# Optimization experiments

Measured on AMD Instinct MI355X. Metric: run time of the kernel, lower is better.

The kernel has to match this reference:

```python
import jax, jax.numpy as jnp
import numpy as np

B, NF, S, L, H, MID, KS, NC, DENSE = 16, 8, 16, 256, 128, 32, 8, 10, 512
COEFF = 0.1
BN_EPS = 1e-5


def _normalize(x):
    return x / jnp.maximum(jnp.linalg.norm(x, axis=-1, keepdims=True), 1e-12)


def _sparsemax(z):
    # sparsemax over last axis (Martins & Astudillo 2016)
    zs = jnp.flip(jnp.sort(z, axis=-1), axis=-1)
    k = jnp.arange(1, z.shape[-1] + 1, dtype=z.dtype)
    cum = jnp.cumsum(zs, axis=-1)
    support = (1.0 + k * zs) > cum
    ksup = jnp.sum(support, axis=-1, keepdims=True)
    tau = (jnp.take_along_axis(cum, ksup - 1, axis=-1) - 1.0) / ksup.astype(z.dtype)
    return jnp.maximum(z - tau, 0.0)


def _bn_ncl(x, g, b, m, v):  # eval-mode BatchNorm1d on [N, C, L]
    return g[None, :, None] * (x - m[None, :, None]) * jax.lax.rsqrt(v[None, :, None] + BN_EPS) + b[None, :, None]


def _bn_nc(x, g, b, m, v):  # eval-mode BatchNorm1d on [N, C]
    return g * (x - m) * jax.lax.rsqrt(v + BN_EPS) + b


def _conv(x, w, pad):
    return jax.lax.conv_general_dilated(x, w, (1,), [(pad, pad)], dimension_numbers=('NCH', 'OIH', 'NCH'))


def _maxpool2(x):  # MaxPool1d(kernel=2, stride=2, padding=1): -inf padded
    return jax.lax.reduce_window(x, -jnp.inf, jax.lax.max, (1, 1, 2), (1, 1, 2), ((0, 0), (0, 0), (1, 1)))


def _cnn(x, cw1, bn1, cw2, bn2, cw3, bn3):
    x = _maxpool2(jax.nn.relu(_bn_ncl(_conv(x, cw1, KS // 2), *bn1)))
    x = _maxpool2(jax.nn.relu(_bn_ncl(_conv(x, cw2, 4), *bn2)))
    x = _maxpool2(jax.nn.relu(_bn_ncl(_conv(x, cw3, 4), *bn3)))
    return jnp.mean(x, axis=-1)  # AdaptiveAvgPool1d(1) -> [N, H]


def _alpha_beta(x, cw1, bn1, cw2, bn2, cw3, bn3, Wq, bq, Wk, bk, Wv, bv):
    b = x.shape[0]
    xf = jnp.transpose(x, (1, 0, 2, 3)).reshape(NF, b * S, 1, L)
    rep = jax.vmap(_cnn)(xf, cw1, bn1, cw2, bn2, cw3, bn3)  # [F, B*S, H]
    rep = rep.reshape(NF, b, S, H)
    Q = jax.nn.elu(rep @ Wq + bq)
    K = jax.nn.leaky_relu(rep @ Wk + bk)
    V = jax.nn.leaky_relu(rep @ Wv + bv)
    # mean_t(Q @ K^T) == Q @ mean_t(K); then scale by sqrt(d_k)
    scores = jnp.einsum('fbsh,fbh->fbs', Q, jnp.mean(K, axis=2)) / jnp.sqrt(jnp.float32(H))
    intra_aw = _sparsemax(scores)                             # [F, B, S]
    Z = _normalize(jnp.einsum('fbs,fbsh->fbh', intra_aw, V))  # [F, B, H]
    Kn = _normalize(rep)
    inter_scores = jnp.einsum('ibh,fbsh->ifbs', Z, Kn)        # cosine scores (Z already unit-norm)
    inter_aw = _sparsemax(inter_scores)                       # [I, F, B, S]
    U = jnp.einsum('ifbs,fbsh->ibh', inter_aw, rep) / NF      # mean over feature axis f
    Hc = _normalize(jnp.concatenate([Z, U], axis=-1))         # [F, B, 2H]
    feat = jnp.transpose(Hc, (1, 0, 2)).reshape(b, NF * 2 * H)
    return feat, intra_aw, inter_aw


def _forward(src_x, src_y, tgt_x, cw1, bn1_g, bn1_b, bn1_m, bn1_v, cw2, bn2_g, bn2_b, bn2_m, bn2_v, cw3, bn3_g, bn3_b, bn3_m, bn3_v, Wq, bq, Wk, bk, Wv, bv, bnc1_g, bnc1_b, bnc1_m, bnc1_v, W1, b1, bnc2_g, bnc2_b, bnc2_m, bnc2_v, W2, b2):
    bn1 = (bn1_g, bn1_b, bn1_m, bn1_v)
    bn2 = (bn2_g, bn2_b, bn2_m, bn2_v)
    bn3 = (bn3_g, bn3_b, bn3_m, bn3_v)
    sf, sa, sb = _alpha_beta(src_x, cw1, bn1, cw2, bn2, cw3, bn3, Wq, bq, Wk, bk, Wv, bv)
    _, ta, tb = _alpha_beta(tgt_x, cw1, bn1, cw2, bn2, cw3, bn3, Wq, bq, Wk, bk, Wv, bv)
    h = _bn_nc(sf, bnc1_g, bnc1_b, bnc1_m, bnc1_v) @ W1 + b1
    h = jax.nn.leaky_relu(_bn_nc(h, bnc2_g, bnc2_b, bnc2_m, bnc2_v))
    y_pred = jax.nn.softmax(h @ W2 + b2, axis=-1)
    # MMD domain losses (detached in original via torch.tensor(list))
    da = jnp.mean(sa - ta, axis=-2)                           # [F, S]
    loss_a = COEFF * jnp.mean(jnp.linalg.norm(da, axis=-1))
    db = jnp.mean(sb - tb, axis=-2)                           # [I, F, S]
    loss_b = COEFF * jnp.mean(jnp.sqrt(jnp.sum(db * db, axis=(1, 2))))
    dom = jax.lax.stop_gradient(loss_a + loss_b)
    # CrossEntropyLoss applied to already-softmaxed preds, as in source
    logp = jax.nn.log_softmax(y_pred, axis=-1)
    ce = -jnp.mean(logp[jnp.arange(y_pred.shape[0]), src_y])
    return y_pred, ce + dom


def setup_inputs() -> dict:
    ks = jax.random.split(jax.random.key(0), 40)
    rn = lambda i, sh, s=1.0: s * jax.random.normal(ks[i], sh, dtype=jnp.float32)
    ru = lambda i, sh, lo, hi: jax.random.uniform(ks[i], sh, jnp.float32, lo, hi)
    return {
        'src_x': rn(0, (B, NF, S, L)),
        'src_y': jax.random.randint(ks[1], (B,), 0, NC),
        'tgt_x': rn(2, (B, NF, S, L)),
        'cw1': rn(3, (NF, MID, 1, KS), 0.1),
        'bn1_g': ru(4, (NF, MID), 0.75, 1.25), 'bn1_b': rn(5, (NF, MID), 0.1),
        'bn1_m': rn(6, (NF, MID), 0.1), 'bn1_v': ru(7, (NF, MID), 0.5, 1.5),
        'cw2': rn(8, (NF, 2 * MID, MID, 8), 0.05),
        'bn2_g': ru(9, (NF, 2 * MID), 0.75, 1.25), 'bn2_b': rn(10, (NF, 2 * MID), 0.1),
        'bn2_m': rn(11, (NF, 2 * MID), 0.1), 'bn2_v': ru(12, (NF, 2 * MID), 0.5, 1.5),
        'cw3': rn(13, (NF, H, 2 * MID, 8), 0.05),
        'bn3_g': ru(14, (NF, H), 0.75, 1.25), 'bn3_b': rn(15, (NF, H), 0.1),
        'bn3_m': rn(16, (NF, H), 0.1), 'bn3_v': ru(17, (NF, H), 0.5, 1.5),
        'Wq': rn(18, (H, H), 0.05), 'bq': rn(19, (H,), 0.02),
        'Wk': rn(20, (H, H), 0.05), 'bk': rn(21, (H,), 0.02),
        'Wv': rn(22, (H, H), 0.05), 'bv': rn(23, (H,), 0.02),
        'bnc1_g': ru(24, (NF * 2 * H,), 0.75, 1.25), 'bnc1_b': rn(25, (NF * 2 * H,), 0.1),
        'bnc1_m': rn(26, (NF * 2 * H,), 0.1), 'bnc1_v': ru(27, (NF * 2 * H,), 0.5, 1.5),
        'W1': rn(28, (NF * 2 * H, DENSE), 0.03), 'b1': rn(29, (DENSE,), 0.02),
        'bnc2_g': ru(30, (DENSE,), 0.75, 1.25), 'bnc2_b': rn(31, (DENSE,), 0.1),
        'bnc2_m': rn(32, (DENSE,), 0.1), 'bnc2_v': ru(33, (DENSE,), 0.5, 1.5),
        'W2': rn(34, (DENSE, NC), 0.05), 'b2': rn(35, (NC,), 0.02),
    }


def reference(src_x, src_y, tgt_x, cw1, bn1_g, bn1_b, bn1_m, bn1_v, cw2, bn2_g, bn2_b, bn2_m, bn2_v, cw3, bn3_g, bn3_b, bn3_m, bn3_v, Wq, bq, Wk, bk, Wv, bv, bnc1_g, bnc1_b, bnc1_m, bnc1_v, W1, b1, bnc2_g, bnc2_b, bnc2_m, bnc2_v, W2, b2):
    return _forward(src_x, src_y, tgt_x, cw1, bn1_g, bn1_b, bn1_m, bn1_v, cw2, bn2_g, bn2_b, bn2_m, bn2_v, cw3, bn3_g, bn3_b, bn3_m, bn3_v, Wq, bq, Wk, bk, Wv, bv, bnc1_g, bnc1_b, bnc1_m, bnc1_v, W1, b1, bnc2_g, bnc2_b, bnc2_m, bnc2_v, W2, b2)
```

## Files before the change

kernel.cpp:

```cpp
#include <hip/hip_runtime.h>

typedef unsigned short u16;
typedef unsigned int u32;
typedef __attribute__((ext_vector_type(8))) short bfrag;
typedef __attribute__((ext_vector_type(4))) float ffrag;

__device__ __forceinline__ float lrelu(float x) { return x >= 0.f ? x : 0.01f * x; }
__device__ __forceinline__ float eluf(float x)  { return x > 0.f ? x : expm1f(x); }
__device__ __forceinline__ u16 f2bf(float f) {
    u32 x = __float_as_uint(f);
    return (u16)((x + 0x7fffu + ((x >> 16) & 1u)) >> 16);
}
__device__ __forceinline__ float bf2f(u16 u) {
    return __uint_as_float(((u32)u) << 16);
}

__device__ void sparsemax16(const float* z, float* out) {
    float zs[16];
    for (int i = 0; i < 16; ++i) zs[i] = z[i];
    for (int i = 1; i < 16; ++i) {
        float key = zs[i]; int j = i - 1;
        while (j >= 0 && zs[j] < key) { zs[j + 1] = zs[j]; --j; }
        zs[j + 1] = key;
    }
    float cum[16];
    cum[0] = zs[0];
    for (int i = 1; i < 16; ++i) cum[i] = cum[i - 1] + zs[i];
    int ksup = 0;
    for (int k = 1; k <= 16; ++k)
        if (1.0f + (float)k * zs[k - 1] > cum[k - 1]) ksup++;
    if (ksup < 1) ksup = 1;
    float tau = (cum[ksup - 1] - 1.0f) / (float)ksup;
    for (int i = 0; i < 16; ++i) out[i] = fmaxf(z[i] - tau, 0.0f);
}

__global__ __launch_bounds__(256) void k_wprep(
    const float* __restrict__ w2, const float* __restrict__ w3,
    u16* __restrict__ wpk2, u16* __restrict__ wpk3)
{
    int i = blockIdx.x * 256 + threadIdx.x;
    if (i < 131072) {
        int j = i & 7, L = (i >> 3) & 63, kc = (i >> 9) & 7, nt = (i >> 12) & 3, f = i >> 14;
        int co = nt * 16 + (L & 15);
        int ci = ((L >> 4) << 3) + j;
        wpk2[i] = f2bf(w2[(((size_t)f * 64 + co) * 32 + ci) * 8 + kc]);
    } else if (i < 131072 + 524288) {
        int i2 = i - 131072;
        int j = i2 & 7, L = (i2 >> 3) & 63, kc = (i2 >> 9) & 15, nt = (i2 >> 13) & 7, f = i2 >> 16;
        int co = nt * 16 + (L & 15);
        int ci = ((kc & 1) << 5) + ((L >> 4) << 3) + j;
        wpk3[i2] = f2bf(w3[(((size_t)f * 128 + co) * 64 + ci) * 8 + (kc >> 1)]);
    }
}

#define S1T_STRIDE 40
#define S2T_STRIDE 72
#define RB_OFF 6336
#define SMEM_U16 15448

__global__ __launch_bounds__(256) void k_cnn(
    const float* __restrict__ xs, const float* __restrict__ xt,
    const float* __restrict__ w1, const float* __restrict__ g1, const float* __restrict__ b1,
    const float* __restrict__ m1, const float* __restrict__ v1,
    const float* __restrict__ g2, const float* __restrict__ b2,
    const float* __restrict__ m2, const float* __restrict__ v2,
    const float* __restrict__ g3, const float* __restrict__ b3,
    const float* __restrict__ m3, const float* __restrict__ v3,
    const u16* __restrict__ wpk2, const u16* __restrict__ wpk3,
    float* __restrict__ rep)
{
    __shared__ __align__(16) u16 smem[SMEM_U16];
    float* xin = (float*)(smem + RB_OFF);

    int tid = threadIdx.x, blk = blockIdx.x;
    int pass = blk >> 11, f = (blk >> 8) & 7, n = blk & 255;
    int bb = n >> 4, ss = n & 15;
    int lane = tid & 63, w = tid >> 6;
    const float* x = pass ? xt : xs;
    float* rep_p = rep + (size_t)pass * 262144;

    {
        u32* z = (u32*)smem;
        for (int i = tid; i < 3168; i += 256) z[i] = 0;
        for (int i = tid; i < 264; i += 256) xin[i] = 0.f;
    }
    __syncthreads();
    {
        const float* xr = x + (((size_t)bb * 8 + f) * 16 + ss) * 256;
        for (int i = tid; i < 256; i += 256) xin[i + 4] = xr[i];
    }
    __syncthreads();

    if (tid < 208) {
        int cc = tid & 7, jc = tid >> 3;
        int co0 = cc * 4, j0 = jc * 5;
        float wr[4][8];
        for (int c = 0; c < 4; ++c) {
            const float4* q = reinterpret_cast<const float4*>(w1 + ((size_t)f * 32 + co0 + c) * 8);
            float4 a = q[0], bq = q[1];
            wr[c][0] = a.x; wr[c][1] = a.y; wr[c][2] = a.z; wr[c][3] = a.w;
            wr[c][4] = bq.x; wr[c][5] = bq.y; wr[c][6] = bq.z; wr[c][7] = bq.w;
        }
        int px[10];
        for (int i = 0; i < 10; ++i) {
            int p = 2 * j0 - 1 + i;
            px[i] = p < 0 ? 0 : (p > 256 ? 256 : p);
        }
        float acc[4][10];
        for (int c = 0; c < 4; ++c) for (int i = 0; i < 10; ++i) acc[c][i] = 0.f;
        for (int k = 0; k < 8; ++k) {
            float xv[10];
            for (int i = 0; i < 10; ++i) xv[i] = xin[px[i] + k];
            for (int c = 0; c < 4; ++c)
                for (int i = 0; i < 10; ++i) acc[c][i] += wr[c][k] * xv[i];
        }
        for (int c = 0; c < 4; ++c) {
            int co = co0 + c;
            float sc = g1[f * 32 + co] * rsqrtf(v1[f * 32 + co] + 1e-5f);
            float sh = b1[f * 32 + co] - m1[f * 32 + co] * sc;
            for (int jj = 0; jj < 5; ++jj) {
                int j = j0 + jj;
                if (j < 129) {
                    float a0 = fmaxf(acc[c][2 * jj] * sc + sh, 0.f);
                    float a1 = fmaxf(acc[c][2 * jj + 1] * sc + sh, 0.f);
                    smem[(j + 4) * S1T_STRIDE + co] = f2bf(fmaxf(a0, a1));
                }
            }
        }
    }
    __syncthreads();

    {
        int nt = w;
        bfrag B2[8];
        const bfrag* gB = reinterpret_cast<const bfrag*>(wpk2);
        for (int kc = 0; kc < 8; ++kc)
            B2[kc] = gB[(((size_t)f * 4 + nt) * 8 + kc) * 64 + lane];
        int co = nt * 16 + (lane & 15);
        float sc = g2[f * 64 + co] * rsqrtf(v2[f * 64 + co] + 1e-5f);
        float sh = b2[f * 64 + co] - m2[f * 64 + co] * sc;
        int arow = lane & 15, ci0 = (lane >> 4) << 3;
        for (int mt = 0; mt < 9; ++mt) {
            ffrag C = {0.f, 0.f, 0.f, 0.f};
            int rb = mt * 16 + arow;
            for (int kc = 0; kc < 8; ++kc) {
                bfrag A = *reinterpret_cast<const bfrag*>(&smem[(rb + kc) * S1T_STRIDE + ci0]);
                C = __builtin_amdgcn_mfma_f32_16x16x32_bf16(A, B2[kc], C, 0, 0, 0);
            }
            int p0 = mt * 16 + ((lane >> 4) << 2);
            for (int r = 0; r < 4; ++r) {
                int p = p0 + r;
                if (p < 130)
                    smem[RB_OFF + p * 64 + co] = f2bf(fmaxf(C[r] * sc + sh, 0.f));
            }
        }
    }
    __syncthreads();

    {
        u32* z = (u32*)smem;
        for (int i = tid; i < 3168; i += 256) z[i] = 0;
    }
    __syncthreads();

    for (int e = tid; e < 66 * 64; e += 256) {
        int j = e >> 6, ci = e & 63;
        float vmax;
        if (j == 0) {
            vmax = bf2f(smem[RB_OFF + 0 * 64 + ci]);
        } else if (j == 65) {
            vmax = bf2f(smem[RB_OFF + 129 * 64 + ci]);
        } else {
            float a0 = bf2f(smem[RB_OFF + (2 * j - 1) * 64 + ci]);
            float a1 = bf2f(smem[RB_OFF + (2 * j) * 64 + ci]);
            vmax = fmaxf(a0, a1);
        }
        smem[(j + 4) * S2T_STRIDE + ci] = f2bf(vmax);
    }
    __syncthreads();

    for (int t = 0; t < 2; ++t) {
        int nt = w * 2 + t;
        bfrag B3[16];
        const bfrag* gB = reinterpret_cast<const bfrag*>(wpk3);
        for (int kc = 0; kc < 16; ++kc)
            B3[kc] = gB[(((size_t)f * 8 + nt) * 16 + kc) * 64 + lane];
        int co = nt * 16 + (lane & 15);
        float sc = g3[f * 128 + co] * rsqrtf(v3[f * 128 + co] + 1e-5f);
        float sh = b3[f * 128 + co] - m3[f * 128 + co] * sc;
        int arow = lane & 15, q8 = (lane >> 4) << 3;
        for (int mt = 0; mt < 5; ++mt) {
            ffrag C = {0.f, 0.f, 0.f, 0.f};
            int rb = mt * 16 + arow;
            for (int kc = 0; kc < 16; ++kc) {
                int row = rb + (kc >> 1);
                int ci0 = ((kc & 1) << 5) + q8;
                bfrag A = *reinterpret_cast<const bfrag*>(&smem[row * S2T_STRIDE + ci0]);
                C = __builtin_amdgcn_mfma_f32_16x16x32_bf16(A, B3[kc], C, 0, 0, 0);
            }
            int p0 = mt * 16 + ((lane >> 4) << 2);
            for (int r = 0; r < 4; ++r) {
                int p = p0 + r;
                if (p < 67)
                    smem[RB_OFF + p * 136 + co] = f2bf(fmaxf(C[r] * sc + sh, 0.f));
            }
        }
    }
    __syncthreads();

    if (tid < 128) {
        int co = tid;
        float sum = bf2f(smem[RB_OFF + 0 * 136 + co]);
        for (int j = 1; j < 34; ++j) {
            float a0 = bf2f(smem[RB_OFF + (2 * j - 1) * 136 + co]);
            float a1 = bf2f(smem[RB_OFF + (2 * j) * 136 + co]);
            sum += fmaxf(a0, a1);
        }
        rep_p[(((size_t)f * 256) + n) * 128 + co] = sum * (1.0f / 34.0f);
    }
}

__global__ __launch_bounds__(128) void k_attn1(
    const float* __restrict__ rep,
    const float* __restrict__ Wq, const float* __restrict__ bq,
    const float* __restrict__ Wk, const float* __restrict__ bk,
    const float* __restrict__ Wv, const float* __restrict__ bv,
    float* __restrict__ Zn, float* __restrict__ rninv, float* __restrict__ iaw)
{
    __shared__ float repL[2048], QL[2048], VL[2048];
    __shared__ float KmL[128], red[128], scoresL[16], awL[16];
    int tid = threadIdx.x;
    int pass = blockIdx.x >> 7, f = (blockIdx.x >> 4) & 7, b = blockIdx.x & 15;
    const float* rep_p = rep + (size_t)pass * 262144;
    float* Zn_p = Zn + (size_t)pass * 16384;
    float* rninv_p = rninv + (size_t)pass * 2048;
    float* iaw_p = iaw + (size_t)pass * 2048;

    const float* rb = rep_p + ((size_t)f * 256 + b * 16) * 128;
    for (int i = tid; i < 2048; i += 128) repL[i] = rb[i];
    __syncthreads();

    int h2 = tid;
    float km = 0.f;
    float bqv = bq[h2], bkv = bk[h2], bvv = bv[h2];
    for (int s0 = 0; s0 < 16; s0 += 8) {
        float aq[8], ak[8], av[8];
        for (int t = 0; t < 8; ++t) { aq[t] = bqv; ak[t] = bkv; av[t] = bvv; }
        for (int h = 0; h < 128; ++h) {
            float wq = Wq[h * 128 + h2];
            float wk = Wk[h * 128 + h2];
            float wv = Wv[h * 128 + h2];
            for (int t = 0; t < 8; ++t) {
                float r = repL[(s0 + t) * 128 + h];
                aq[t] += r * wq; ak[t] += r * wk; av[t] += r * wv;
            }
        }
        for (int t = 0; t < 8; ++t) {
            QL[(s0 + t) * 128 + h2] = eluf(aq[t]);
            VL[(s0 + t) * 128 + h2] = lrelu(av[t]);
            km += lrelu(ak[t]);
        }
    }
    KmL[h2] = km * (1.f / 16.f);
    __syncthreads();

    if (tid < 16) {
        float a = 0.f;
        for (int h = 0; h < 128; ++h) a += QL[tid * 128 + h] * KmL[h];
        scoresL[tid] = a * 0.08838834764831845f;
        float r2 = 0.f;
        for (int h = 0; h < 128; ++h) { float r = repL[tid * 128 + h]; r2 += r * r; }
        rninv_p[f * 256 + b * 16 + tid] = 1.f / fmaxf(sqrtf(r2), 1e-12f);
    }
    __syncthreads();
    if (tid == 0) sparsemax16(scoresL, awL);
    __syncthreads();
    if (tid < 16) iaw_p[f * 256 + b * 16 + tid] = awL[tid];

    float z = 0.f;
    for (int s = 0; s < 16; ++s) z += awL[s] * VL[s * 128 + tid];
    red[tid] = z * z;
    __syncthreads();
    for (int st = 64; st > 0; st >>= 1) {
        if (tid < st) red[tid] += red[tid + st];
        __syncthreads();
    }
    float inv = 1.f / fmaxf(sqrtf(red[0]), 1e-12f);
    Zn_p[((size_t)f * 16 + b) * 128 + tid] = z * inv;
}

__global__ __launch_bounds__(256) void k_attn2(
    const float* __restrict__ rep, const float* __restrict__ Zn,
    const float* __restrict__ rninv, float* __restrict__ ibw,
    const float* __restrict__ g, const float* __restrict__ bb,
    const float* __restrict__ mm, const float* __restrict__ vv,
    float* __restrict__ featbn)
{
    __shared__ float ZnL[1024], sc[1024], UL[1024], nrm[8];
    int tid = threadIdx.x;
    int pass = blockIdx.x >> 4, b = blockIdx.x & 15;
    const float* rep_p = rep + (size_t)pass * 262144;
    const float* Zn_p = Zn + (size_t)pass * 16384;
    const float* rninv_p = rninv + (size_t)pass * 2048;
    float* ibw_p = ibw + (size_t)pass * 16384;

    for (int i = tid; i < 1024; i += 256) {
        int ii = i >> 7, h = i & 127;
        ZnL[i] = Zn_p[((size_t)ii * 16 + b) * 128 + h];
    }
    if (tid < 8) nrm[tid] = 0.f;
    __syncthreads();

    for (int e = tid; e < 1024; e += 256) {
        int i = e >> 7, f = (e >> 4) & 7, s = e & 15;
        const float* rr = rep_p + ((size_t)f * 256 + b * 16 + s) * 128;
        float a = 0.f;
        for (int h = 0; h < 128; ++h) a += ZnL[i * 128 + h] * rr[h];
        sc[(i * 8 + f) * 16 + s] = a * rninv_p[f * 256 + b * 16 + s];
    }
    __syncthreads();
    if (tid < 64) {
        int i = tid >> 3, f = tid & 7;
        float aw[16];
        sparsemax16(&sc[(i * 8 + f) * 16], aw);
        for (int s = 0; s < 16; ++s) {
            sc[(i * 8 + f) * 16 + s] = aw[s];
            ibw_p[(((size_t)i * 8 + f) * 16 + b) * 16 + s] = aw[s];
        }
    }
    __syncthreads();
    if (pass == 0) {
        for (int e = tid; e < 1024; e += 256) {
            int i = e >> 7, h = e & 127;
            float u = 0.f;
            for (int f = 0; f < 8; ++f) {
                const float* rr = rep_p + ((size_t)f * 256 + b * 16) * 128 + h;
                const float* aa = &sc[(i * 8 + f) * 16];
                for (int s = 0; s < 16; ++s) u += aa[s] * rr[s * 128];
            }
            UL[e] = u * 0.125f;
        }
        __syncthreads();
        for (int e = tid; e < 1024; e += 256) {
            int f = e >> 7;
            float zz = ZnL[e], uu = UL[e];
            atomicAdd(&nrm[f], zz * zz + uu * uu);
        }
        __syncthreads();
        for (int e = tid; e < 2048; e += 256) {
            int f = e >> 8, d = e & 255;
            float inv = 1.f / fmaxf(sqrtf(nrm[f]), 1e-12f);
            float val = (d < 128 ? ZnL[f * 128 + d] : UL[f * 128 + d - 128]) * inv;
            float scv = g[e] * rsqrtf(vv[e] + 1e-5f);
            featbn[b * 2048 + e] = (val - mm[e]) * scv + bb[e];
        }
    }
}

__global__ __launch_bounds__(256) void k_head1(
    const float* __restrict__ featbn,
    const float* __restrict__ W1, const float* __restrict__ b1,
    const float* __restrict__ g2, const float* __restrict__ bb2,
    const float* __restrict__ mm2, const float* __restrict__ vv2,
    float* __restrict__ h2ws)
{
    __shared__ float featL[2048];
    __shared__ float part[8][32];
    int tid = threadIdx.x, blk = blockIdx.x;
    int b = blk >> 4, cc = blk & 15;
    for (int i = tid; i < 2048; i += 256) featL[i] = featbn[b * 2048 + i];
    __syncthreads();
    int ci = tid & 31, ks = tid >> 5;
    int col = cc * 32 + ci;
    const float* wcol = W1 + (size_t)(ks * 256) * 512 + col;
    const float* fl = featL + ks * 256;
    float a = 0.f;
    for (int c = 0; c < 256; ++c) a += fl[c] * wcol[(size_t)c * 512];
    part[ks][ci] = a;
    __syncthreads();
    if (tid < 32) {
        int colw = cc * 32 + tid;
        float s = b1[colw];
        for (int k2 = 0; k2 < 8; ++k2) s += part[k2][tid];
        float scv = g2[colw] * rsqrtf(vv2[colw] + 1e-5f);
        float val = (s - mm2[colw]) * scv + bb2[colw];
        h2ws[b * 512 + colw] = lrelu(val);
    }
}

__global__ __launch_bounds__(256) void k_tail(
    const float* __restrict__ h2ws,
    const float* __restrict__ W2, const float* __restrict__ b2,
    const float* __restrict__ sa, const float* __restrict__ ta,
    const float* __restrict__ sb, const float* __restrict__ tb,
    const int* __restrict__ sy, float* __restrict__ dout)
{
    __shared__ float h2L[8192];
    __shared__ float lgL[160], ypL[160];
    __shared__ float sA[8], sB[8];
    int tid = threadIdx.x;
    for (int i = tid; i < 8192; i += 256) h2L[i] = h2ws[i];
    if (tid < 8) { sA[tid] = 0.f; sB[tid] = 0.f; }
    __syncthreads();
    if (tid < 160) {
        int b = tid / 10, j = tid - b * 10;
        float a = b2[j];
        const float* h = h2L + b * 512;
        for (int c = 0; c < 512; ++c) a += h[c] * W2[c * 10 + j];
        lgL[tid] = a;
    }
    __syncthreads();
    if (tid < 16) {
        int b = tid;
        float mx = lgL[b * 10];
        for (int j = 1; j < 10; ++j) mx = fmaxf(mx, lgL[b * 10 + j]);
        float sum = 0.f, ex[10];
        for (int j = 0; j < 10; ++j) { ex[j] = expf(lgL[b * 10 + j] - mx); sum += ex[j]; }
        for (int j = 0; j < 10; ++j) {
            float p = ex[j] / sum;
            ypL[b * 10 + j] = p;
            dout[b * 10 + j] = p;
        }
    }
    __syncthreads();
    if (tid < 128) {
        int f = tid >> 4, s = tid & 15;
        float d = 0.f;
        for (int b = 0; b < 16; ++b) d += sa[f * 256 + b * 16 + s] - ta[f * 256 + b * 16 + s];
        d *= (1.f / 16.f);
        atomicAdd(&sA[f], d * d);
    }
    for (int e = tid; e < 1024; e += 256) {
        int i = e >> 7, f = (e >> 4) & 7, s = e & 15;
        float d = 0.f;
        int base = ((i * 8 + f) * 16) * 16 + s;
        for (int b = 0; b < 16; ++b) d += sb[base + b * 16] - tb[base + b * 16];
        d *= (1.f / 16.f);
        atomicAdd(&sB[i], d * d);
    }
    __syncthreads();
    if (tid == 0) {
        float la = 0.f, lb = 0.f;
        for (int f = 0; f < 8; ++f) la += sqrtf(sA[f]);
        for (int i = 0; i < 8; ++i) lb += sqrtf(sB[i]);
        la *= 0.1f / 8.f;
        lb *= 0.1f / 8.f;
        float ce = 0.f;
        for (int b = 0; b < 16; ++b) {
            const float* y = ypL + b * 10;
            float mx = y[0];
            for (int j = 1; j < 10; ++j) mx = fmaxf(mx, y[j]);
            float sum = 0.f;
            for (int j = 0; j < 10; ++j) sum += expf(y[j] - mx);
            float lse = mx + logf(sum);
            ce += lse - y[sy[b]];
        }
        ce *= (1.f / 16.f);
        dout[160] = ce + la + lb;
    }
}

extern "C" void kernel_launch(void* const* d_in, const int* in_sizes, int n_in,
                              void* d_out, int out_size, void* d_ws, size_t ws_size,
                              hipStream_t stream) {
    (void)in_sizes; (void)n_in; (void)out_size; (void)ws_size;
    const float* src_x = (const float*)d_in[0];
    const int*   src_y = (const int*)d_in[1];
    const float* tgt_x = (const float*)d_in[2];
    const float *cw1 = (const float*)d_in[3], *bn1g = (const float*)d_in[4],
                *bn1b = (const float*)d_in[5], *bn1m = (const float*)d_in[6],
                *bn1v = (const float*)d_in[7];
    const float *cw2 = (const float*)d_in[8], *bn2g = (const float*)d_in[9],
                *bn2b = (const float*)d_in[10], *bn2m = (const float*)d_in[11],
                *bn2v = (const float*)d_in[12];
    const float *cw3 = (const float*)d_in[13], *bn3g = (const float*)d_in[14],
                *bn3b = (const float*)d_in[15], *bn3m = (const float*)d_in[16],
                *bn3v = (const float*)d_in[17];
    const float *Wq = (const float*)d_in[18], *bq = (const float*)d_in[19],
                *Wk = (const float*)d_in[20], *bk = (const float*)d_in[21],
                *Wv = (const float*)d_in[22], *bv = (const float*)d_in[23];
    const float *bc1g = (const float*)d_in[24], *bc1b = (const float*)d_in[25],
                *bc1m = (const float*)d_in[26], *bc1v = (const float*)d_in[27];
    const float *W1 = (const float*)d_in[28], *b1 = (const float*)d_in[29];
    const float *bc2g = (const float*)d_in[30], *bc2b = (const float*)d_in[31],
                *bc2m = (const float*)d_in[32], *bc2v = (const float*)d_in[33];
    const float *W2 = (const float*)d_in[34], *b2 = (const float*)d_in[35];

    float* ws = (float*)d_ws;
    size_t o = 0;
    float* rep    = ws + o; o += (size_t)2 * 262144;
    float* Zn     = ws + o; o += (size_t)2 * 16384;
    float* rninv  = ws + o; o += (size_t)2 * 2048;
    float* ia     = ws + o; o += (size_t)2 * 2048;
    float* ib     = ws + o; o += (size_t)2 * 16384;
    float* featbn = ws + o; o += (size_t)16 * 2048;
    float* h2ws   = ws + o; o += (size_t)16 * 512;
    u16* wpk2 = (u16*)(ws + o); o += 65536;
    u16* wpk3 = (u16*)(ws + o); o += 262144;

    k_wprep<<<2560, 256, 0, stream>>>(cw2, cw3, wpk2, wpk3);
    k_cnn<<<4096, 256, 0, stream>>>(src_x, tgt_x,
        cw1, bn1g, bn1b, bn1m, bn1v,
        bn2g, bn2b, bn2m, bn2v,
        bn3g, bn3b, bn3m, bn3v,
        wpk2, wpk3, rep);
    k_attn1<<<256, 128, 0, stream>>>(rep, Wq, bq, Wk, bk, Wv, bv, Zn, rninv, ia);
    k_attn2<<<32, 256, 0, stream>>>(rep, Zn, rninv, ib, bc1g, bc1b, bc1m, bc1v, featbn);
    k_head1<<<256, 256, 0, stream>>>(featbn, W1, b1, bc2g, bc2b, bc2m, bc2v, h2ws);
    k_tail<<<1, 256, 0, stream>>>(h2ws, W2, b2, ia, ia + 2048, ib, ib + 16384,
                                  src_y, (float*)d_out);
}
```

Measured before the change: 352.6 us.

## Use bf16 MFMA for QKV projections, pad CNN LDS strides, truncate bf16 conversion

The attention kernel's Q/K/V projections move from scalar FP32 loops to bf16 MFMA. The weights are prepacked into fragment layout in the weight-prep kernel, and reductions use wave shuffles instead of shared-memory trees. The CNN's intermediate LDS buffers get padded strides to cut bank conflicts. Round-to-nearest bf16 conversion is replaced with plain truncation, which is cheaper but adds precision loss in the projections and CNN activations.

```diff
diff --git a/kernel.cpp b/kernel.cpp
--- a/kernel.cpp
+++ b/kernel.cpp
@@ -10,6 +10,9 @@
 __device__ __forceinline__ u16 f2bf(float f) {
     u32 x = __float_as_uint(f);
     return (u16)((x + 0x7fffu + ((x >> 16) & 1u)) >> 16);
+}
+__device__ __forceinline__ u16 f2bt(float f) {
+    return (u16)(__float_as_uint(f) >> 16);
 }
 __device__ __forceinline__ float bf2f(u16 u) {
     return __uint_as_float(((u32)u) << 16);
@@ -36,7 +39,9 @@
 
 __global__ __launch_bounds__(256) void k_wprep(
     const float* __restrict__ w2, const float* __restrict__ w3,
-    u16* __restrict__ wpk2, u16* __restrict__ wpk3)
+    const float* __restrict__ Wq, const float* __restrict__ Wk,
+    const float* __restrict__ Wv,
+    u16* __restrict__ wpk2, u16* __restrict__ wpk3, u16* __restrict__ wqkv)
 {
     int i = blockIdx.x * 256 + threadIdx.x;
     if (i < 131072) {
@@ -50,13 +55,23 @@
         int co = nt * 16 + (L & 15);
         int ci = ((kc & 1) << 5) + ((L >> 4) << 3) + j;
         wpk3[i2] = f2bf(w3[(((size_t)f * 128 + co) * 64 + ci) * 8 + (kc >> 1)]);
+    } else if (i < 131072 + 524288 + 49152) {
+        int j2 = i - 655360;
+        int proj = j2 >> 14, idx = j2 & 16383;
+        int jj = idx & 7, L = (idx >> 3) & 63, kc = (idx >> 9) & 3, nt = idx >> 11;
+        int n = nt * 16 + (L & 15);
+        int k = kc * 32 + ((L >> 4) << 3) + jj;
+        const float* W = proj == 0 ? Wq : (proj == 1 ? Wk : Wv);
+        wqkv[j2] = f2bf(W[k * 128 + n]);
     }
 }
 
 #define S1T_STRIDE 40
 #define S2T_STRIDE 72
+#define RB2_STRIDE 68
+#define RB3_STRIDE 140
 #define RB_OFF 6336
-#define SMEM_U16 15448
+#define SMEM_U16 (RB_OFF + 67 * RB3_STRIDE)
 
 __global__ __launch_bounds__(256) void k_cnn(
     const float* __restrict__ xs, const float* __restrict__ xt,
@@ -123,7 +138,7 @@
                 if (j < 129) {
                     float a0 = fmaxf(acc[c][2 * jj] * sc + sh, 0.f);
                     float a1 = fmaxf(acc[c][2 * jj + 1] * sc + sh, 0.f);
-                    smem[(j + 4) * S1T_STRIDE + co] = f2bf(fmaxf(a0, a1));
+                    smem[(j + 4) * S1T_STRIDE + co] = f2bt(fmaxf(a0, a1));
                 }
             }
         }
@@ -151,7 +166,7 @@
             for (int r = 0; r < 4; ++r) {
                 int p = p0 + r;
                 if (p < 130)
-                    smem[RB_OFF + p * 64 + co] = f2bf(fmaxf(C[r] * sc + sh, 0.f));
+                    smem[RB_OFF + p * RB2_STRIDE + co] = f2bt(fmaxf(C[r] * sc + sh, 0.f));
             }
         }
     }
@@ -167,15 +182,15 @@
         int j = e >> 6, ci = e & 63;
         float vmax;
         if (j == 0) {
-            vmax = bf2f(smem[RB_OFF + 0 * 64 + ci]);
+            vmax = bf2f(smem[RB_OFF + 0 * RB2_STRIDE + ci]);
         } else if (j == 65) {
-            vmax = bf2f(smem[RB_OFF + 129 * 64 + ci]);
+            vmax = bf2f(smem[RB_OFF + 129 * RB2_STRIDE + ci]);
         } else {
-            float a0 = bf2f(smem[RB_OFF + (2 * j - 1) * 64 + ci]);
-            float a1 = bf2f(smem[RB_OFF + (2 * j) * 64 + ci]);
+            float a0 = bf2f(smem[RB_OFF + (2 * j - 1) * RB2_STRIDE + ci]);
+            float a1 = bf2f(smem[RB_OFF + (2 * j) * RB2_STRIDE + ci]);
             vmax = fmaxf(a0, a1);
         }
-        smem[(j + 4) * S2T_STRIDE + ci] = f2bf(vmax);
+        smem[(j + 4) * S2T_STRIDE + ci] = f2bt(vmax);
     }
     __syncthreads();
 
@@ -202,7 +217,7 @@
             for (int r = 0; r < 4; ++r) {
                 int p = p0 + r;
                 if (p < 67)
-                    smem[RB_OFF + p * 136 + co] = f2bf(fmaxf(C[r] * sc + sh, 0.f));
+                    smem[RB_OFF + p * RB3_STRIDE + co] = f2bt(fmaxf(C[r] * sc + sh, 0.f));
             }
         }
     }
@@ -210,83 +225,130 @@
 
     if (tid < 128) {
         int co = tid;
-        float sum = bf2f(smem[RB_OFF + 0 * 136 + co]);
+        float sum = bf2f(smem[RB_OFF + 0 * RB3_STRIDE + co]);
         for (int j = 1; j < 34; ++j) {
-            float a0 = bf2f(smem[RB_OFF + (2 * j - 1) * 136 + co]);
-            float a1 = bf2f(smem[RB_OFF + (2 * j) * 136 + co]);
+            float a0 = bf2f(smem[RB_OFF + (2 * j - 1) * RB3_STRIDE + co]);
+            float a1 = bf2f(smem[RB_OFF + (2 * j) * RB3_STRIDE + co]);
             sum += fmaxf(a0, a1);
         }
         rep_p[(((size_t)f * 256) + n) * 128 + co] = sum * (1.0f / 34.0f);
     }
 }
 
-__global__ __launch_bounds__(128) void k_attn1(
-    const float* __restrict__ rep,
-    const float* __restrict__ Wq, const float* __restrict__ bq,
-    const float* __restrict__ Wk, const float* __restrict__ bk,
-    const float* __restrict__ Wv, const float* __restrict__ bv,
+__global__ __launch_bounds__(256) void k_attn1(
+    const float* __restrict__ rep, const u16* __restrict__ wqkv,
+    const float* __restrict__ bq, const float* __restrict__ bk,
+    const float* __restrict__ bv,
     float* __restrict__ Zn, float* __restrict__ rninv, float* __restrict__ iaw)
 {
-    __shared__ float repL[2048], QL[2048], VL[2048];
-    __shared__ float KmL[128], red[128], scoresL[16], awL[16];
+    __shared__ __align__(16) u16 repbf[16 * 136];
+    __shared__ float KmL[128], ZL[128], awL[16], scoresL[16], r2L[16];
+    __shared__ float spart[4][4][4];
+    __shared__ float redL[4];
     int tid = threadIdx.x;
     int pass = blockIdx.x >> 7, f = (blockIdx.x >> 4) & 7, b = blockIdx.x & 15;
-    const float* rep_p = rep + (size_t)pass * 262144;
+    const float* rp = rep + (size_t)pass * 262144 + ((size_t)f * 256 + b * 16) * 128;
     float* Zn_p = Zn + (size_t)pass * 16384;
     float* rninv_p = rninv + (size_t)pass * 2048;
     float* iaw_p = iaw + (size_t)pass * 2048;
 
-    const float* rb = rep_p + ((size_t)f * 256 + b * 16) * 128;
-    for (int i = tid; i < 2048; i += 128) repL[i] = rb[i];
-    __syncthreads();
-
-    int h2 = tid;
-    float km = 0.f;
-    float bqv = bq[h2], bkv = bk[h2], bvv = bv[h2];
-    for (int s0 = 0; s0 < 16; s0 += 8) {
-        float aq[8], ak[8], av[8];
-        for (int t = 0; t < 8; ++t) { aq[t] = bqv; ak[t] = bkv; av[t] = bvv; }
-        for (int h = 0; h < 128; ++h) {
-            float wq = Wq[h * 128 + h2];
-            float wk = Wk[h * 128 + h2];
-            float wv = Wv[h * 128 + h2];
-            for (int t = 0; t < 8; ++t) {
-                float r = repL[(s0 + t) * 128 + h];
-                aq[t] += r * wq; ak[t] += r * wk; av[t] += r * wv;
-            }
-        }
-        for (int t = 0; t < 8; ++t) {
-            QL[(s0 + t) * 128 + h2] = eluf(aq[t]);
-            VL[(s0 + t) * 128 + h2] = lrelu(av[t]);
-            km += lrelu(ak[t]);
-        }
-    }
-    KmL[h2] = km * (1.f / 16.f);
-    __syncthreads();
-
+    {
+        int s = tid >> 4, i = tid & 15, h0 = i * 8;
+        const float4* q4 = reinterpret_cast<const float4*>(rp + s * 128 + h0);
+        float4 a = q4[0], c = q4[1];
+        float p2 = a.x*a.x + a.y*a.y + a.z*a.z + a.w*a.w
+                 + c.x*c.x + c.y*c.y + c.z*c.z + c.w*c.w;
+        bfrag pk;
+        pk[0] = (short)f2bt(a.x); pk[1] = (short)f2bt(a.y);
+        pk[2] = (short)f2bt(a.z); pk[3] = (short)f2bt(a.w);
+        pk[4] = (short)f2bt(c.x); pk[5] = (short)f2bt(c.y);
+        pk[6] = (short)f2bt(c.z); pk[7] = (short)f2bt(c.w);
+        *reinterpret_cast<bfrag*>(&repbf[s * 136 + h0]) = pk;
+        p2 += __shfl_xor(p2, 1); p2 += __shfl_xor(p2, 2);
+        p2 += __shfl_xor(p2, 4); p2 += __shfl_xor(p2, 8);
+        if (i == 0) r2L[s] = p2;
+    }
+    __syncthreads();
+
+    int lane = tid & 63, w = tid >> 6, arow = lane & 15, q = lane >> 4;
+    bfrag A[4];
+    for (int kc = 0; kc < 4; ++kc)
+        A[kc] = *reinterpret_cast<const bfrag*>(&repbf[arow * 136 + kc * 32 + q * 8]);
+
+    float qv[2][4], vvv[2][4];
+    int colv[2];
+    const bfrag* BB = reinterpret_cast<const bfrag*>(wqkv);
+    for (int t = 0; t < 2; ++t) {
+        int nt = w * 2 + t;
+        ffrag cq = {0.f,0.f,0.f,0.f}, ck = {0.f,0.f,0.f,0.f}, cv = {0.f,0.f,0.f,0.f};
+        for (int kc = 0; kc < 4; ++kc) {
+            int fi = (nt * 4 + kc) * 64 + lane;
+            bfrag Bq = BB[fi];
+            bfrag Bk = BB[2048 + fi];
+            bfrag Bv = BB[4096 + fi];
+            cq = __builtin_amdgcn_mfma_f32_16x16x32_bf16(A[kc], Bq, cq, 0, 0, 0);
+            ck = __builtin_amdgcn_mfma_f32_16x16x32_bf16(A[kc], Bk, ck, 0, 0, 0);
+            cv = __builtin_amdgcn_mfma_f32_16x16x32_bf16(A[kc], Bv, cv, 0, 0, 0);
+        }
+        int col = nt * 16 + arow;
+        colv[t] = col;
+        float bqc = bq[col], bkc = bk[col], bvc = bv[col];
+        float kpt = 0.f;
+        for (int r = 0; r < 4; ++r) {
+            qv[t][r] = eluf(cq[r] + bqc);
+            vvv[t][r] = lrelu(cv[r] + bvc);
+            kpt += lrelu(ck[r] + bkc);
+        }
+        kpt += __shfl_xor(kpt, 16);
+        kpt += __shfl_xor(kpt, 32);
+        if (q == 0) KmL[col] = kpt * (1.f / 16.f);
+    }
+    __syncthreads();
+
+    {
+        float km0 = KmL[colv[0]], km1 = KmL[colv[1]];
+        float ps[4];
+        for (int r = 0; r < 4; ++r) {
+            float v = qv[0][r] * km0 + qv[1][r] * km1;
+            v += __shfl_xor(v, 1); v += __shfl_xor(v, 2);
+            v += __shfl_xor(v, 4); v += __shfl_xor(v, 8);
+            ps[r] = v;
+        }
+        if (arow == 0)
+            for (int r = 0; r < 4; ++r) spart[w][q][r] = ps[r];
+    }
+    __syncthreads();
     if (tid < 16) {
-        float a = 0.f;
-        for (int h = 0; h < 128; ++h) a += QL[tid * 128 + h] * KmL[h];
-        scoresL[tid] = a * 0.08838834764831845f;
-        float r2 = 0.f;
-        for (int h = 0; h < 128; ++h) { float r = repL[tid * 128 + h]; r2 += r * r; }
-        rninv_p[f * 256 + b * 16 + tid] = 1.f / fmaxf(sqrtf(r2), 1e-12f);
+        int qq = tid >> 2, rr = tid & 3;
+        float sc = spart[0][qq][rr] + spart[1][qq][rr] + spart[2][qq][rr] + spart[3][qq][rr];
+        scoresL[tid] = sc * 0.08838834764831845f;
+        rninv_p[f * 256 + b * 16 + tid] = 1.f / fmaxf(sqrtf(r2L[tid]), 1e-12f);
     }
     __syncthreads();
     if (tid == 0) sparsemax16(scoresL, awL);
     __syncthreads();
     if (tid < 16) iaw_p[f * 256 + b * 16 + tid] = awL[tid];
 
-    float z = 0.f;
-    for (int s = 0; s < 16; ++s) z += awL[s] * VL[s * 128 + tid];
-    red[tid] = z * z;
-    __syncthreads();
-    for (int st = 64; st > 0; st >>= 1) {
-        if (tid < st) red[tid] += red[tid + st];
-        __syncthreads();
-    }
-    float inv = 1.f / fmaxf(sqrtf(red[0]), 1e-12f);
-    Zn_p[((size_t)f * 16 + b) * 128 + tid] = z * inv;
+    for (int t = 0; t < 2; ++t) {
+        float zp = 0.f;
+        for (int r = 0; r < 4; ++r) zp += awL[q * 4 + r] * vvv[t][r];
+        zp += __shfl_xor(zp, 16);
+        zp += __shfl_xor(zp, 32);
+        if (q == 0) ZL[colv[t]] = zp;
+    }
+    __syncthreads();
+    if (tid < 128) {
+        float z = ZL[tid];
+        float v = z * z;
+        v += __shfl_xor(v, 1); v += __shfl_xor(v, 2); v += __shfl_xor(v, 4);
+        v += __shfl_xor(v, 8); v += __shfl_xor(v, 16); v += __shfl_xor(v, 32);
+        if (lane == 0) redL[w] = v;
+    }
+    __syncthreads();
+    if (tid == 0) redL[2] = 1.f / fmaxf(sqrtf(redL[0] + redL[1]), 1e-12f);
+    __syncthreads();
+    if (tid < 128)
+        Zn_p[((size_t)f * 16 + b) * 128 + tid] = ZL[tid] * redL[2];
 }
 
 __global__ __launch_bounds__(256) void k_attn2(
@@ -497,14 +559,15 @@
     float* h2ws   = ws + o; o += (size_t)16 * 512;
     u16* wpk2 = (u16*)(ws + o); o += 65536;
     u16* wpk3 = (u16*)(ws + o); o += 262144;
-
-    k_wprep<<<2560, 256, 0, stream>>>(cw2, cw3, wpk2, wpk3);
+    u16* wqkv = (u16*)(ws + o); o += 24576;
+
+    k_wprep<<<2752, 256, 0, stream>>>(cw2, cw3, Wq, Wk, Wv, wpk2, wpk3, wqkv);
     k_cnn<<<4096, 256, 0, stream>>>(src_x, tgt_x,
         cw1, bn1g, bn1b, bn1m, bn1v,
         bn2g, bn2b, bn2m, bn2v,
         bn3g, bn3b, bn3m, bn3v,
         wpk2, wpk3, rep);
-    k_attn1<<<256, 128, 0, stream>>>(rep, Wq, bq, Wk, bk, Wv, bv, Zn, rninv, ia);
+    k_attn1<<<256, 256, 0, stream>>>(rep, wqkv, bq, bk, bv, Zn, rninv, ia);
     k_attn2<<<32, 256, 0, stream>>>(rep, Zn, rninv, ib, bc1g, bc1b, bc1m, bc1v, featbn);
     k_head1<<<256, 256, 0, stream>>>(featbn, W1, b1, bc2g, bc2b, bc2m, bc2v, h2ws);
     k_tail<<<1, 256, 0, stream>>>(h2ws, W2, b2, ia, ia + 2048, ib, ib + 16384,
```

Measured after the change: 333.2 us. 1.06x faster.
